# Kernel optimization log

Hardware: AMD Instinct MI355X
Metric: run time of the kernel (lower is better)

Reference implementation:

```python
import jax, jax.numpy as jnp
import numpy as np

B, C, H, W = 8, 128, 64, 64

def setup_inputs() -> dict:
    key = jax.random.key(0)
    ks = jax.random.split(key, 8)
    s = 1.0 / np.sqrt(C)
    return {
        "x": jax.random.normal(ks[0], (B, C, H, W), dtype=jnp.float32),
        "dw_q": jax.random.normal(ks[1], (C,), dtype=jnp.float32) * s,
        "pw_q": jax.random.normal(ks[2], (C, C), dtype=jnp.float32) * s,
        "dw_k": jax.random.normal(ks[3], (C,), dtype=jnp.float32) * s,
        "pw_k": jax.random.normal(ks[4], (C, C), dtype=jnp.float32) * s,
        "dw_v": jax.random.normal(ks[5], (C,), dtype=jnp.float32) * s,
        "pw_v": jax.random.normal(ks[6], (C, C), dtype=jnp.float32) * s,
        "gamma": jnp.zeros((1,), dtype=jnp.float32) + 0.5,
    }

def _proj(x, dw, pw):
    # depthwise 1x1 (groups=C, no bias) == per-channel scale; then pointwise 1x1 conv (C_out=C)
    xs = x * dw[None, :, None, None]
    return jnp.einsum('oc,bchw->bohw', pw, xs)

def reference(x, dw_q, pw_q, dw_k, pw_k, dw_v, pw_v, gamma):
    b, c, h, w = x.shape
    n = h * w
    q = _proj(x, dw_q, pw_q).reshape(b, c, n)   # B,C,N
    k = _proj(x, dw_k, pw_k).reshape(b, c, n)
    v = _proj(x, dw_v, pw_v).reshape(b, c, n)
    # energy[b,n,m] = sum_c q[b,c,n] k[b,c,m]  (no scaling, as in source)
    energy = jnp.einsum('bcn,bcm->bnm', q, k)
    attn = jax.nn.softmax(energy, axis=-1)      # B,N,N
    # out[b,c,n] = sum_m v[b,c,m] attn[b,n,m]
    out = jnp.einsum('bcm,bnm->bcn', v, attn).reshape(b, c, h, w)
    return gamma[0] * out + x
```

## Files before the change

kernel.cpp:

```cpp
#include <hip/hip_runtime.h>
#include <hip/hip_bf16.h>


typedef __bf16 v8bf __attribute__((ext_vector_type(8)));
typedef float  v4f  __attribute__((ext_vector_type(4)));

#define B_ 8
#define C_ 128
#define N_ 4096

static __device__ __forceinline__ unsigned short f2bf_rne(float f) {
    union { float f; unsigned u; } v; v.f = f;
    return (unsigned short)((v.u + 0x7fffu + ((v.u >> 16) & 1u)) >> 16);
}
static __device__ __forceinline__ unsigned fbits(float f) {
    union { float f; unsigned u; } v; v.f = f; return v.u;
}

__global__ __launch_bounds__(256, 2) void proj_kernel(
    const float* __restrict__ x,
    const float* __restrict__ dw_q, const float* __restrict__ pw_q,
    const float* __restrict__ dw_k, const float* __restrict__ pw_k,
    const float* __restrict__ dw_v, const float* __restrict__ pw_v,
    unsigned short* __restrict__ qf_ws, unsigned short* __restrict__ kt,
    unsigned short* __restrict__ vt)
{
    __shared__ unsigned short xT[128 * 136];
    __shared__ unsigned short Ws[128 * 136];

    const int bid = blockIdx.x;
    const int bb  = bid & 7;
    const int t   = (bid >> 3) & 31;
    const int pp  = bid >> 8;
    const int n0  = t * 128;
    const int tid = threadIdx.x;
    const int w    = tid >> 6;
    const int lane = tid & 63;
    const int quad = lane >> 4;
    const int l16  = lane & 15;

    #pragma unroll
    for (int k = 0; k < 16; ++k) {
        const int idx = tid + k * 256;
        const int c  = idx >> 5;
        const int nq = idx & 31;
        float4 f = *(const float4*)(x + ((size_t)(bb * C_ + c)) * N_ + n0 + nq * 4);
        xT[(nq * 4 + 0) * 136 + c] = f2bf_rne(f.x);
        xT[(nq * 4 + 1) * 136 + c] = f2bf_rne(f.y);
        xT[(nq * 4 + 2) * 136 + c] = f2bf_rne(f.z);
        xT[(nq * 4 + 3) * 136 + c] = f2bf_rne(f.w);
    }
    const float* pw = (pp == 0) ? pw_q : (pp == 1) ? pw_k : pw_v;
    const float* dw = (pp == 0) ? dw_q : (pp == 1) ? dw_k : dw_v;
    const float qs = (pp == 0) ? 1.4426950408889634f : 1.0f;
    #pragma unroll
    for (int k = 0; k < 16; ++k) {
        const int idx = tid + k * 256;
        const int o  = idx >> 5;
        const int c4 = (idx & 31) * 4;
        float4 p4 = *(const float4*)(pw + o * 128 + c4);
        float4 d4 = *(const float4*)(dw + c4);
        unsigned lo = (unsigned)f2bf_rne(p4.x * d4.x * qs) | ((unsigned)f2bf_rne(p4.y * d4.y * qs) << 16);
        unsigned hi = (unsigned)f2bf_rne(p4.z * d4.z * qs) | ((unsigned)f2bf_rne(p4.w * d4.w * qs) << 16);
        *(unsigned long long*)&Ws[o * 136 + c4] =
            (unsigned long long)lo | ((unsigned long long)hi << 32);
    }
    __syncthreads();

    const unsigned short* As = (pp < 2) ? xT : Ws;
    const unsigned short* Bs = (pp < 2) ? Ws : xT;

    v4f acc[2][8];
    #pragma unroll
    for (int i = 0; i < 2; ++i)
        #pragma unroll
        for (int j = 0; j < 8; ++j)
            acc[i][j] = (v4f){0.f, 0.f, 0.f, 0.f};

    #pragma unroll
    for (int kc = 0; kc < 4; ++kc) {
        v8bf av[2];
        #pragma unroll
        for (int i = 0; i < 2; ++i)
            av[i] = *(const v8bf*)&As[(w * 32 + i * 16 + l16) * 136 + kc * 32 + quad * 8];
        #pragma unroll
        for (int cb = 0; cb < 8; ++cb) {
            v8bf bv = *(const v8bf*)&Bs[(cb * 16 + l16) * 136 + kc * 32 + quad * 8];
            acc[0][cb] = __builtin_amdgcn_mfma_f32_16x16x32_bf16(av[0], bv, acc[0][cb], 0, 0, 0);
            acc[1][cb] = __builtin_amdgcn_mfma_f32_16x16x32_bf16(av[1], bv, acc[1][cb], 0, 0, 0);
        }
    }
    __syncthreads();

    unsigned short* sc = Ws;
    #pragma unroll
    for (int mi = 0; mi < 2; ++mi)
        #pragma unroll
        for (int cb = 0; cb < 8; ++cb)
            #pragma unroll
            for (int r = 0; r < 4; ++r)
                sc[(w * 32 + mi * 16 + quad * 4 + r) * 136 + cb * 16 + l16] =
                    f2bf_rne(acc[mi][cb][r]);
    __syncthreads();

    if (pp == 0) {
        unsigned short* dst = qf_ws + ((size_t)(bb * 64 + t * 2)) * 8192;
        #pragma unroll
        for (int p = 0; p < 8; ++p) {
            const int g     = p * 4 + w;
            const int strip = g >> 4, ni = (g >> 2) & 3, kc = g & 3;
            *(uint4*)(dst + ((size_t)g * 64 + lane) * 8) =
                *(const uint4*)&sc[(strip * 64 + ni * 16 + l16) * 136 + kc * 32 + quad * 8];
        }
    } else if (pp == 1) {
        unsigned short* dst = kt + ((size_t)(bb * 32 + t)) * 16384;
        #pragma unroll
        for (int p = 0; p < 8; ++p) {
            const int g  = p * 4 + w;
            const int mb = g >> 2, kc = g & 3;
            *(uint4*)(dst + ((size_t)g * 64 + lane) * 8) =
                *(const uint4*)&sc[(mb * 16 + l16) * 136 + kc * 32 + quad * 8];
        }
    } else {
        unsigned short* dst = vt + ((size_t)(bb * 32 + t)) * 16384;
        #pragma unroll
        for (int p = 0; p < 8; ++p) {
            const int d  = p * 256 + tid;
            const int cb = d >> 8, wq = (d >> 4) & 15, l = d & 15;
            *(uint4*)(dst + (size_t)d * 8) =
                *(const uint4*)&sc[(cb * 16 + l) * 136 + wq * 8];
        }
    }
}

#define MFMA(A, B, C) __builtin_amdgcn_mfma_f32_16x16x32_bf16(A, B, C, 0, 0, 0)
#define EXP2(X) __builtin_amdgcn_exp2f(X)
#define PKPERM(EH, EL) __builtin_amdgcn_perm(fbits(EH), fbits(EL), 0x07060302)

#define LOADK(KF, TILE) { \
    const unsigned short* kp_ = kbase + (size_t)(TILE) * 16384; \
    _Pragma("unroll") \
    for (int mi_ = 0; mi_ < 2; ++mi_) \
        _Pragma("unroll") \
        for (int kc_ = 0; kc_ < 4; ++kc_) \
            KF[mi_][kc_] = *(const v8bf*)(kp_ + (size_t)((mi_ * 4 + kc_) * 64) * 8); \
}

#define LOADV(TILE) { \
    const unsigned short* vp_ = vbase + (size_t)(TILE) * 16384; \
    _Pragma("unroll") \
    for (int cb_ = 0; cb_ < 8; ++cb_) \
        vf[cb_] = *(const v8bf*)(vp_ + (size_t)(cb_ * 256) * 8); \
}

#define MKPF(NI, PK0A, PK0B, PK1A, PK1B) { \
    unsigned sLo_ = (quad < 2) ? PK0A : PK1A; \
    unsigned sHi_ = (quad < 2) ? PK0B : PK1B; \
    union { unsigned u[4]; v8bf v; } pu_; \
    pu_.u[0] = (unsigned)__builtin_amdgcn_ds_bpermute(la, (int)sLo_); \
    pu_.u[1] = (unsigned)__builtin_amdgcn_ds_bpermute(la, (int)sHi_); \
    pu_.u[2] = (unsigned)__builtin_amdgcn_ds_bpermute(lb, (int)sLo_); \
    pu_.u[3] = (unsigned)__builtin_amdgcn_ds_bpermute(lb, (int)sHi_); \
    pf[NI] = pu_.v; \
}

#define SCOMP0(KF, SC) { \
    _Pragma("unroll") \
    for (int mi_ = 0; mi_ < 2; ++mi_) \
        _Pragma("unroll") \
        for (int ni_ = 0; ni_ < 2; ++ni_) { \
            v4f a_ = MFMA(KF[mi_][0], qf[ni_][0], Z4v); \
            _Pragma("unroll") \
            for (int kc_ = 1; kc_ < 4; ++kc_) \
                a_ = MFMA(KF[mi_][kc_], qf[ni_][kc_], a_); \
            SC[mi_][ni_] = a_; \
        } \
}

#define FUSED(SC_IN, KF, SC_OUT) { \
    float e0_, e1_, e2_, e3_; \
    unsigned pk00a_, pk00b_, pk10a_, pk10b_, pk01a_, pk01b_, pk11a_, pk11b_; \
     \
    SC_OUT[0][0] = MFMA(KF[0][0], qf[0][0], Z4v); \
    SC_OUT[0][1] = MFMA(KF[0][0], qf[1][0], Z4v); \
    e0_ = EXP2(SC_IN[0][0][0]); e1_ = EXP2(SC_IN[0][0][1]); \
    e2_ = EXP2(SC_IN[0][0][2]); e3_ = EXP2(SC_IN[0][0][3]); \
     \
    SC_OUT[0][0] = MFMA(KF[0][1], qf[0][1], SC_OUT[0][0]); \
    SC_OUT[0][1] = MFMA(KF[0][1], qf[1][1], SC_OUT[0][1]); \
    lpart[0] += (e0_ + e1_) + (e2_ + e3_); \
    pk00a_ = PKPERM(e1_, e0_); pk00b_ = PKPERM(e3_, e2_); \
     \
    SC_OUT[0][0] = MFMA(KF[0][2], qf[0][2], SC_OUT[0][0]); \
    SC_OUT[0][1] = MFMA(KF[0][2], qf[1][2], SC_OUT[0][1]); \
    e0_ = EXP2(SC_IN[1][0][0]); e1_ = EXP2(SC_IN[1][0][1]); \
    e2_ = EXP2(SC_IN[1][0][2]); e3_ = EXP2(SC_IN[1][0][3]); \
     \
    SC_OUT[0][0] = MFMA(KF[0][3], qf[0][3], SC_OUT[0][0]); \
    SC_OUT[0][1] = MFMA(KF[0][3], qf[1][3], SC_OUT[0][1]); \
    lpart[0] += (e0_ + e1_) + (e2_ + e3_); \
    pk10a_ = PKPERM(e1_, e0_); pk10b_ = PKPERM(e3_, e2_); \
     \
    SC_OUT[1][0] = MFMA(KF[1][0], qf[0][0], Z4v); \
    SC_OUT[1][1] = MFMA(KF[1][0], qf[1][0], Z4v); \
    MKPF(0, pk00a_, pk00b_, pk10a_, pk10b_) \
     \
    SC_OUT[1][0] = MFMA(KF[1][1], qf[0][1], SC_OUT[1][0]); \
    SC_OUT[1][1] = MFMA(KF[1][1], qf[1][1], SC_OUT[1][1]); \
    e0_ = EXP2(SC_IN[0][1][0]); e1_ = EXP2(SC_IN[0][1][1]); \
    e2_ = EXP2(SC_IN[0][1][2]); e3_ = EXP2(SC_IN[0][1][3]); \
     \
    SC_OUT[1][0] = MFMA(KF[1][2], qf[0][2], SC_OUT[1][0]); \
    SC_OUT[1][1] = MFMA(KF[1][2], qf[1][2], SC_OUT[1][1]); \
    lpart[1] += (e0_ + e1_) + (e2_ + e3_); \
    pk01a_ = PKPERM(e1_, e0_); pk01b_ = PKPERM(e3_, e2_); \
     \
    SC_OUT[1][0] = MFMA(KF[1][3], qf[0][3], SC_OUT[1][0]); \
    SC_OUT[1][1] = MFMA(KF[1][3], qf[1][3], SC_OUT[1][1]); \
    e0_ = EXP2(SC_IN[1][1][0]); e1_ = EXP2(SC_IN[1][1][1]); \
    e2_ = EXP2(SC_IN[1][1][2]); e3_ = EXP2(SC_IN[1][1][3]); \
    lpart[1] += (e0_ + e1_) + (e2_ + e3_); \
    pk11a_ = PKPERM(e1_, e0_); pk11b_ = PKPERM(e3_, e2_); \
    MKPF(1, pk01a_, pk01b_, pk11a_, pk11b_) \
}

#define PVOP { \
    _Pragma("unroll") \
    for (int ni_ = 0; ni_ < 2; ++ni_) \
        _Pragma("unroll") \
        for (int cb_ = 0; cb_ < 8; ++cb_) \
            oacc[cb_][ni_] = MFMA(vf[cb_], pf[ni_], oacc[cb_][ni_]); \
}

__global__ __launch_bounds__(256, 2) void attn_kernel(
    const unsigned short* __restrict__ qf_ws, const unsigned short* __restrict__ kt,
    const unsigned short* __restrict__ vt, const float* __restrict__ x,
    const float* __restrict__ gamma, float* __restrict__ out)
{
    __shared__ float red[32 * 132];
    __shared__ float l_s[4][32];

    const int bid = blockIdx.x;
    const int bb  = bid & 7;
    const int s   = bid >> 3;
    const int n0  = s * 32;
    const int tid = threadIdx.x;
    const int w    = tid >> 6;
    const int lane = tid & 63;
    const int quad = lane >> 4;
    const int l16  = lane & 15;

    v8bf qf[2][4];
    {
        const unsigned short* qb = qf_ws + ((size_t)(bb * 128 + s)) * 4096;
        #pragma unroll
        for (int ni = 0; ni < 2; ++ni)
            #pragma unroll
            for (int kc = 0; kc < 4; ++kc)
                qf[ni][kc] = *(const v8bf*)(qb + ((size_t)(ni * 4 + kc) * 64 + lane) * 8);
    }

    v4f oacc[8][2];
    #pragma unroll
    for (int i = 0; i < 8; ++i)
        #pragma unroll
        for (int j = 0; j < 2; ++j)
            oacc[i][j] = (v4f){0.f, 0.f, 0.f, 0.f};
    float lpart[2] = {0.f, 0.f};
    const v4f Z4v = {0.f, 0.f, 0.f, 0.f};

    const int la = ((((quad & 1) << 1) << 4) + l16) << 2;
    const int lb = la + 64;

    const unsigned short* kbase = kt + ((size_t)(bb * 32)) * 16384 + ((size_t)(w * 8) * 64 + lane) * 8;
    const unsigned short* vbase = vt + ((size_t)(bb * 32)) * 16384 + ((size_t)(w * 64 + lane)) * 8;

    v8bf kfA[2][4], kfB[2][4], vf[8];
    v4f sc0[2][2], sc1[2][2];
    v8bf pf[2];

    LOADK(kfA, 0)
    LOADV(0)
    LOADK(kfB, 1)
    SCOMP0(kfA, sc0)

    for (int it = 0; it < 32; it += 2) {
        LOADK(kfA, (it + 2) & 31)
        FUSED(sc0, kfB, sc1)
        PVOP
        LOADV((it + 1) & 31)
        LOADK(kfB, (it + 3) & 31)
        FUSED(sc1, kfA, sc0)
        PVOP
        LOADV((it + 2) & 31)
    }

    #pragma unroll
    for (int ni = 0; ni < 2; ++ni) {
        float r = lpart[ni];
        r += __shfl_xor(r, 16);
        r += __shfl_xor(r, 32);
        if (lane < 16) l_s[w][ni * 16 + lane] = r;
    }

    for (int rw = 0; rw < 4; ++rw) {
        if (w == rw) {
            #pragma unroll
            for (int cb = 0; cb < 8; ++cb)
                #pragma unroll
                for (int ni = 0; ni < 2; ++ni) {
                    float* p = &red[(ni * 16 + l16) * 132 + cb * 16 + quad * 4];
                    if (rw == 0) *(v4f*)p = oacc[cb][ni];
                    else {
                        v4f tv = *(const v4f*)p;
                        tv += oacc[cb][ni];
                        *(v4f*)p = tv;
                    }
                }
        }
        __syncthreads();
    }

    const float g = gamma[0];
    const int   n = tid & 31;
    const int  cg = tid >> 5;
    const float li = 1.0f / (((l_s[0][n] + l_s[1][n]) + (l_s[2][n] + l_s[3][n])));
    #pragma unroll
    for (int j = 0; j < 16; ++j) {
        const int c = cg * 16 + j;
        const size_t idx = ((size_t)(bb * C_ + c)) * N_ + n0 + n;
        out[idx] = g * red[n * 132 + c] * li + x[idx];
    }
}

extern "C" void kernel_launch(void* const* d_in, const int* in_sizes, int n_in,
                              void* d_out, int out_size, void* d_ws, size_t ws_size,
                              hipStream_t stream)
{
    (void)in_sizes; (void)n_in; (void)out_size; (void)ws_size;
    const float* x     = (const float*)d_in[0];
    const float* dw_q  = (const float*)d_in[1];
    const float* pw_q  = (const float*)d_in[2];
    const float* dw_k  = (const float*)d_in[3];
    const float* pw_k  = (const float*)d_in[4];
    const float* dw_v  = (const float*)d_in[5];
    const float* pw_v  = (const float*)d_in[6];
    const float* gamma = (const float*)d_in[7];
    float* out = (float*)d_out;

    unsigned short* qf_ws = (unsigned short*)d_ws;
    unsigned short* kt    = qf_ws + (size_t)B_ * N_ * C_;
    unsigned short* vt    = kt    + (size_t)B_ * N_ * C_;

    proj_kernel<<<dim3(768), dim3(256), 0, stream>>>(
        x, dw_q, pw_q, dw_k, pw_k, dw_v, pw_v, qf_ws, kt, vt);
    attn_kernel<<<dim3(1024), dim3(256), 0, stream>>>(
        qf_ws, kt, vt, x, gamma, out);
}
```

Measured before the change: 178.9 us.

## Stage V tiles through LDS with async global_load_lds double buffering

```diff
diff --git a/kernel.cpp b/kernel.cpp
--- a/kernel.cpp
+++ b/kernel.cpp
@@ -146,12 +146,26 @@
             KF[mi_][kc_] = *(const v8bf*)(kp_ + (size_t)((mi_ * 4 + kc_) * 64) * 8); \
 }
 
-#define LOADV(TILE) { \
-    const unsigned short* vp_ = vbase + (size_t)(TILE) * 16384; \
+#define STAGE_V(TILE, BUF) { \
+    const unsigned short* vp_ = vstage + (size_t)(TILE) * 16384; \
     _Pragma("unroll") \
     for (int cb_ = 0; cb_ < 8; ++cb_) \
-        vf[cb_] = *(const v8bf*)(vp_ + (size_t)(cb_ * 256) * 8); \
-}
+        __builtin_amdgcn_global_load_lds( \
+            (const __attribute__((address_space(1))) void*)(vp_ + cb_ * 2048), \
+            (__attribute__((address_space(3))) void*)&sm.v[BUF][w][cb_][0], \
+            16, 0, 0); \
+}
+
+#define VLOAD(BUF) { \
+    _Pragma("unroll") \
+    for (int cb_ = 0; cb_ < 8; ++cb_) \
+        vv[cb_] = *(const v8bf*)&sm.v[BUF][w][cb_][lane * 8]; \
+}
+
+#define VWAIT { asm volatile("s_waitcnt vmcnt(16)" ::: "memory"); \
+                __builtin_amdgcn_sched_barrier(0); }
+#define LDRAIN { asm volatile("s_waitcnt lgkmcnt(0)" ::: "memory"); \
+                 __builtin_amdgcn_sched_barrier(0); }
 
 #define MKPF(NI, PK0A, PK0B, PK1A, PK1B) { \
     unsigned sLo_ = (quad < 2) ? PK0A : PK1A; \
@@ -180,41 +194,33 @@
 #define FUSED(SC_IN, KF, SC_OUT) { \
     float e0_, e1_, e2_, e3_; \
     unsigned pk00a_, pk00b_, pk10a_, pk10b_, pk01a_, pk01b_, pk11a_, pk11b_; \
-     \
     SC_OUT[0][0] = MFMA(KF[0][0], qf[0][0], Z4v); \
     SC_OUT[0][1] = MFMA(KF[0][0], qf[1][0], Z4v); \
     e0_ = EXP2(SC_IN[0][0][0]); e1_ = EXP2(SC_IN[0][0][1]); \
     e2_ = EXP2(SC_IN[0][0][2]); e3_ = EXP2(SC_IN[0][0][3]); \
-     \
     SC_OUT[0][0] = MFMA(KF[0][1], qf[0][1], SC_OUT[0][0]); \
     SC_OUT[0][1] = MFMA(KF[0][1], qf[1][1], SC_OUT[0][1]); \
     lpart[0] += (e0_ + e1_) + (e2_ + e3_); \
     pk00a_ = PKPERM(e1_, e0_); pk00b_ = PKPERM(e3_, e2_); \
-     \
     SC_OUT[0][0] = MFMA(KF[0][2], qf[0][2], SC_OUT[0][0]); \
     SC_OUT[0][1] = MFMA(KF[0][2], qf[1][2], SC_OUT[0][1]); \
     e0_ = EXP2(SC_IN[1][0][0]); e1_ = EXP2(SC_IN[1][0][1]); \
     e2_ = EXP2(SC_IN[1][0][2]); e3_ = EXP2(SC_IN[1][0][3]); \
-     \
     SC_OUT[0][0] = MFMA(KF[0][3], qf[0][3], SC_OUT[0][0]); \
     SC_OUT[0][1] = MFMA(KF[0][3], qf[1][3], SC_OUT[0][1]); \
     lpart[0] += (e0_ + e1_) + (e2_ + e3_); \
     pk10a_ = PKPERM(e1_, e0_); pk10b_ = PKPERM(e3_, e2_); \
-     \
     SC_OUT[1][0] = MFMA(KF[1][0], qf[0][0], Z4v); \
     SC_OUT[1][1] = MFMA(KF[1][0], qf[1][0], Z4v); \
     MKPF(0, pk00a_, pk00b_, pk10a_, pk10b_) \
-     \
     SC_OUT[1][0] = MFMA(KF[1][1], qf[0][1], SC_OUT[1][0]); \
     SC_OUT[1][1] = MFMA(KF[1][1], qf[1][1], SC_OUT[1][1]); \
     e0_ = EXP2(SC_IN[0][1][0]); e1_ = EXP2(SC_IN[0][1][1]); \
     e2_ = EXP2(SC_IN[0][1][2]); e3_ = EXP2(SC_IN[0][1][3]); \
-     \
     SC_OUT[1][0] = MFMA(KF[1][2], qf[0][2], SC_OUT[1][0]); \
     SC_OUT[1][1] = MFMA(KF[1][2], qf[1][2], SC_OUT[1][1]); \
     lpart[1] += (e0_ + e1_) + (e2_ + e3_); \
     pk01a_ = PKPERM(e1_, e0_); pk01b_ = PKPERM(e3_, e2_); \
-     \
     SC_OUT[1][0] = MFMA(KF[1][3], qf[0][3], SC_OUT[1][0]); \
     SC_OUT[1][1] = MFMA(KF[1][3], qf[1][3], SC_OUT[1][1]); \
     e0_ = EXP2(SC_IN[1][1][0]); e1_ = EXP2(SC_IN[1][1][1]); \
@@ -224,12 +230,12 @@
     MKPF(1, pk01a_, pk01b_, pk11a_, pk11b_) \
 }
 
-#define PVOP { \
+#define PVMM { \
     _Pragma("unroll") \
     for (int ni_ = 0; ni_ < 2; ++ni_) \
         _Pragma("unroll") \
         for (int cb_ = 0; cb_ < 8; ++cb_) \
-            oacc[cb_][ni_] = MFMA(vf[cb_], pf[ni_], oacc[cb_][ni_]); \
+            oacc[cb_][ni_] = MFMA(vv[cb_], pf[ni_], oacc[cb_][ni_]); \
 }
 
 __global__ __launch_bounds__(256, 2) void attn_kernel(
@@ -237,7 +243,10 @@
     const unsigned short* __restrict__ vt, const float* __restrict__ x,
     const float* __restrict__ gamma, float* __restrict__ out)
 {
-    __shared__ float red[32 * 132];
+    __shared__ __align__(16) union SMem {
+        unsigned short v[2][4][8][512];
+        float red[32 * 132];
+    } sm;
     __shared__ float l_s[4][32];
 
     const int bid = blockIdx.x;
@@ -272,27 +281,34 @@
     const int la = ((((quad & 1) << 1) << 4) + l16) << 2;
     const int lb = la + 64;
 
-    const unsigned short* kbase = kt + ((size_t)(bb * 32)) * 16384 + ((size_t)(w * 8) * 64 + lane) * 8;
-    const unsigned short* vbase = vt + ((size_t)(bb * 32)) * 16384 + ((size_t)(w * 64 + lane)) * 8;
-
-    v8bf kfA[2][4], kfB[2][4], vf[8];
+    const unsigned short* kbase  = kt + ((size_t)(bb * 32)) * 16384 + ((size_t)(w * 8) * 64 + lane) * 8;
+    const unsigned short* vstage = vt + ((size_t)(bb * 32)) * 16384 + ((size_t)(w * 64 + lane)) * 8;
+
+    v8bf kfA[2][4], kfB[2][4], vv[8];
     v4f sc0[2][2], sc1[2][2];
     v8bf pf[2];
 
     LOADK(kfA, 0)
-    LOADV(0)
+    STAGE_V(0, 0)
     LOADK(kfB, 1)
+    STAGE_V(1, 1)
     SCOMP0(kfA, sc0)
 
     for (int it = 0; it < 32; it += 2) {
         LOADK(kfA, (it + 2) & 31)
+        VWAIT
+        VLOAD(0)
         FUSED(sc0, kfB, sc1)
-        PVOP
-        LOADV((it + 1) & 31)
+        PVMM
+        LDRAIN
+        STAGE_V((it + 2) & 31, 0)
         LOADK(kfB, (it + 3) & 31)
+        VWAIT
+        VLOAD(1)
         FUSED(sc1, kfA, sc0)
-        PVOP
-        LOADV((it + 2) & 31)
+        PVMM
+        LDRAIN
+        STAGE_V((it + 3) & 31, 1)
     }
 
     #pragma unroll
@@ -302,6 +318,8 @@
         r += __shfl_xor(r, 32);
         if (lane < 16) l_s[w][ni * 16 + lane] = r;
     }
+
+    __syncthreads();
 
     for (int rw = 0; rw < 4; ++rw) {
         if (w == rw) {
@@ -309,7 +327,7 @@
             for (int cb = 0; cb < 8; ++cb)
                 #pragma unroll
                 for (int ni = 0; ni < 2; ++ni) {
-                    float* p = &red[(ni * 16 + l16) * 132 + cb * 16 + quad * 4];
+                    float* p = &sm.red[(ni * 16 + l16) * 132 + cb * 16 + quad * 4];
                     if (rw == 0) *(v4f*)p = oacc[cb][ni];
                     else {
                         v4f tv = *(const v4f*)p;
@@ -329,7 +347,7 @@
     for (int j = 0; j < 16; ++j) {
         const int c = cg * 16 + j;
         const size_t idx = ((size_t)(bb * C_ + c)) * N_ + n0 + n;
-        out[idx] = g * red[n * 132 + c] * li + x[idx];
+        out[idx] = g * sm.red[n * 132 + c] * li + x[idx];
     }
 }
 
```

New measurement: 185.1 us. 3.4% more time.
